# Optimization experiments

Hardware: AMD Instinct MI355X
Metric: run time of the kernel (lower is better)

Reference implementation:

```python
import jax, jax.numpy as jnp
import numpy as np

N = 100000
E = 1600000
IN_C = 128
OUT_C = 64
HID = 2 * OUT_C  # 128


def setup_inputs() -> dict:
    key = jax.random.key(0)
    k = jax.random.split(key, 6)
    x = jax.random.normal(k[0], (N, IN_C), dtype=jnp.float32)
    edge_index = jax.random.randint(k[1], (2, E), 0, N, dtype=jnp.int64)
    # GCNConv params (glorot-ish scale)
    W1 = jax.random.normal(k[2], (IN_C, HID), dtype=jnp.float32) / np.sqrt(IN_C)
    b1 = jnp.zeros((HID,), dtype=jnp.float32)
    W2 = jax.random.normal(k[3], (HID, OUT_C), dtype=jnp.float32) / np.sqrt(HID)
    b2 = jnp.zeros((OUT_C,), dtype=jnp.float32)
    return {"x": x, "edge_index": edge_index, "W1": W1, "b1": b1, "W2": W2, "b2": b2}


def _gcn_norm(edge_index, num_nodes):
    # add_self_loops=False: norm over given edges only.
    row, col = edge_index[0], edge_index[1]  # source, target
    deg = jax.ops.segment_sum(jnp.ones((edge_index.shape[1],), jnp.float32), col,
                              num_segments=num_nodes)
    dinv = jnp.where(deg > 0, 1.0 / jnp.sqrt(deg), 0.0)
    return dinv[row] * dinv[col]  # [E]


def _gcn_conv(x, edge_index, norm, W, b):
    row, col = edge_index[0], edge_index[1]
    h = x @ W                                   # [N, D_out] transform first
    msg = h[row] * norm[:, None]                # gather + scale  [E, D_out]
    agg = jax.ops.segment_sum(msg, col, num_segments=x.shape[0])  # scatter-add
    return agg + b


def reference(x, edge_index, W1, b1, W2, b2):
    # Dropout(p=0.9) is identity in eval mode (deterministic baseline).
    norm = _gcn_norm(edge_index, x.shape[0])
    h = _gcn_conv(x, edge_index, norm, W1, b1)
    h = jax.nn.relu(h)
    out = _gcn_conv(h, edge_index, norm, W2, b2)
    return out
```

## Files before the change

### kernel.cpp

```cpp
#include <hip/hip_runtime.h>

#define N_NODES 100000
#define N_EDGES 1600000
#define INC 128
#define HIDC 128
#define OUTC 64

constexpr int BSH = 9;
constexpr int BTGT = 1 << BSH;
constexpr int NBUCK = (N_NODES + BTGT - 1) / BTGT;
constexpr int BCAP = 10240;
constexpr int BIN_TILE = 2048;
constexpr int BIN_EPT = BIN_TILE / 256;
constexpr int NBINBLK = (N_EDGES + BIN_TILE - 1) / BIN_TILE;


__device__ __forceinline__ float blo(unsigned u) { return __uint_as_float(u << 16); }
__device__ __forceinline__ float bhi(unsigned u) { return __uint_as_float(u & 0xFFFF0000u); }
__device__ __forceinline__ unsigned pack_bf2(float a, float b) {
    unsigned ua = __float_as_uint(a);
    ua = (ua + 0x7FFFu + ((ua >> 16) & 1u)) >> 16;
    unsigned ub = __float_as_uint(b);
    ub = (ub + 0x7FFFu + ((ub >> 16) & 1u)) >> 16;
    return ua | (ub << 16);
}


__global__ void k_binit(int* __restrict__ bcur) {
    int b = threadIdx.x;
    if (b < NBUCK) bcur[b] = b * BCAP;
}

__global__ __launch_bounds__(256) void k_bin(const int* __restrict__ ei,
                                             int* __restrict__ bcur,
                                             unsigned* __restrict__ staging) {
    __shared__ int cnt[256];
    __shared__ int base[256];
    const int tid = threadIdx.x;
    cnt[tid] = 0;
    __syncthreads();
    const int e0 = blockIdx.x * BIN_TILE;
    unsigned pk[BIN_EPT];
    int bk[BIN_EPT];
#pragma unroll
    for (int r = 0; r < BIN_EPT; ++r) {
        int e = e0 + r * 256 + tid;
        if (e < N_EDGES) {
            int t = __builtin_nontemporal_load(ei + N_EDGES + e);
            int s = __builtin_nontemporal_load(ei + e);
            bk[r] = t >> BSH;
            pk[r] = ((unsigned)s << BSH) | (unsigned)(t & (BTGT - 1));
            atomicAdd(&cnt[bk[r]], 1);
        } else {
            bk[r] = -1;
        }
    }
    __syncthreads();
    if (tid < NBUCK) {
        int c = cnt[tid];
        base[tid] = (c > 0) ? atomicAdd(&bcur[tid], c) : 0;
    }
    __syncthreads();
#pragma unroll
    for (int r = 0; r < BIN_EPT; ++r) {
        if (bk[r] >= 0) {
            int g = atomicAdd(&base[bk[r]], 1);
            staging[g] = pk[r];
        }
    }
}

__global__ void k_bucket_scan(const int* __restrict__ bcur, int* __restrict__ bbase,
                              int* __restrict__ offs) {
    __shared__ int sdata[256];
    const int tid = threadIdx.x;
    int v = (tid < NBUCK) ? (bcur[tid] - tid * BCAP) : 0;
    sdata[tid] = v;
    __syncthreads();
    for (int off = 1; off < 256; off <<= 1) {
        int t = (tid >= off) ? sdata[tid - off] : 0;
        __syncthreads();
        sdata[tid] += t;
        __syncthreads();
    }
    if (tid < NBUCK) bbase[tid] = sdata[tid] - v;
    if (tid == 0) offs[N_NODES] = N_EDGES;
}

__global__ __launch_bounds__(256) void k_scatter2(const unsigned* __restrict__ staging,
                                                  const int* __restrict__ bcur,
                                                  const int* __restrict__ bbase,
                                                  int* __restrict__ offs,
                                                  float* __restrict__ dinv,
                                                  int* __restrict__ csr_row) {
    __shared__ int cnt[BTGT];
    __shared__ int pos[BTGT];
    __shared__ int sdata[256];
    const int b = blockIdx.x;
    const int tid = threadIdx.x;
    const int segb = b * BCAP;
    const int n = bcur[b] - segb;
    const int g0 = b << BSH;
    const int bb = bbase[b];
    cnt[tid] = 0;
    cnt[tid + 256] = 0;
    __syncthreads();
    for (int j = tid; j < n; j += 256) {
        atomicAdd(&cnt[staging[segb + j] & (BTGT - 1)], 1);
    }
    __syncthreads();
    const int c0 = cnt[2 * tid], c1 = cnt[2 * tid + 1];
    const int s = c0 + c1;
    sdata[tid] = s;
    __syncthreads();
    for (int off = 1; off < 256; off <<= 1) {
        int t = (tid >= off) ? sdata[tid - off] : 0;
        __syncthreads();
        sdata[tid] += t;
        __syncthreads();
    }
    const int texcl = sdata[tid] - s;
    const int o0 = bb + texcl;
    const int o1 = o0 + c0;
    const int gg0 = g0 + 2 * tid, gg1 = g0 + 2 * tid + 1;
    if (gg0 < N_NODES) {
        offs[gg0] = o0;
        dinv[gg0] = (c0 > 0) ? rsqrtf((float)c0) : 0.f;
    }
    if (gg1 < N_NODES) {
        offs[gg1] = o1;
        dinv[gg1] = (c1 > 0) ? rsqrtf((float)c1) : 0.f;
    }
    pos[2 * tid] = o0;
    pos[2 * tid + 1] = o1;
    __syncthreads();
    for (int j = tid; j < n; j += 256) {
        unsigned p = staging[segb + j];
        int lt = p & (BTGT - 1);
        int src = (int)(p >> BSH);
        int pp = atomicAdd(&pos[lt], 1);
        csr_row[pp] = src;
    }
}


template <int BN, int OUTTOT>
__global__ __launch_bounds__(256) void k_gemm3(const float* __restrict__ X,
                                               const float* __restrict__ W,
                                               const float* __restrict__ dinv,
                                               unsigned short* __restrict__ outb) {
    constexpr int OG = OUTTOT / 8;
    constexpr int NG = 256 / OG;
    static_assert(NG * 4 == BN, "tile mismatch");
    constexpr int KC = 32;
    constexpr int HW = OUTTOT / 2;
    constexpr int XITER = (BN * KC) / 1024;
    constexpr int WITER = (KC * OUTTOT) / 1024;

    __shared__ float xs[BN][KC + 4];
    __shared__ float wa[KC][HW];
    __shared__ float wb[KC][HW];

    const int tid = threadIdx.x;
    const int oq = tid % OG;
    const int nq = tid / OG;
    const int n0 = blockIdx.x * BN;
    float acc[4][8] = {};

    for (int kc = 0; kc < 128; kc += KC) {
#pragma unroll
        for (int m = 0; m < XITER; ++m) {
            int q = tid + 256 * m;
            int row = q / (KC / 4);
            int kq = q % (KC / 4);
            int nn = n0 + row;
            float4 v = make_float4(0.f, 0.f, 0.f, 0.f);
            if (nn < N_NODES)
                v = *reinterpret_cast<const float4*>(X + (size_t)nn * 128 + kc + kq * 4);
            *reinterpret_cast<float4*>(&xs[row][kq * 4]) = v;
        }
#pragma unroll
        for (int m = 0; m < WITER; ++m) {
            int q = tid + 256 * m;
            int row = q / (OUTTOT / 4);
            int fq = q % (OUTTOT / 4);
            float4 v = *reinterpret_cast<const float4*>(W + (size_t)(kc + row) * OUTTOT + fq * 4);
            float* dst = (fq & 1) ? &wb[row][(fq >> 1) * 4] : &wa[row][(fq >> 1) * 4];
            *reinterpret_cast<float4*>(dst) = v;
        }
        __syncthreads();
#pragma unroll 8
        for (int k = 0; k < KC; ++k) {
            const float4 w0 = *reinterpret_cast<const float4*>(&wa[k][oq * 4]);
            const float4 w1 = *reinterpret_cast<const float4*>(&wb[k][oq * 4]);
#pragma unroll
            for (int j = 0; j < 4; ++j) {
                float xv = xs[nq + NG * j][k];
                acc[j][0] += xv * w0.x;
                acc[j][1] += xv * w0.y;
                acc[j][2] += xv * w0.z;
                acc[j][3] += xv * w0.w;
                acc[j][4] += xv * w1.x;
                acc[j][5] += xv * w1.y;
                acc[j][6] += xv * w1.z;
                acc[j][7] += xv * w1.w;
            }
        }
        __syncthreads();
    }
#pragma unroll
    for (int j = 0; j < 4; ++j) {
        int nn = n0 + nq + NG * j;
        if (nn < N_NODES) {
            float s = dinv[nn];
            uint4 pkv;
            pkv.x = pack_bf2(acc[j][0] * s, acc[j][1] * s);
            pkv.y = pack_bf2(acc[j][2] * s, acc[j][3] * s);
            pkv.z = pack_bf2(acc[j][4] * s, acc[j][5] * s);
            pkv.w = pack_bf2(acc[j][6] * s, acc[j][7] * s);
            *reinterpret_cast<uint4*>(outb + (size_t)nn * OUTTOT + oq * 8) = pkv;
        }
    }
}


template <int OC, int U, bool RELU>
__global__ __launch_bounds__(256) void k_aggp(const uint4* __restrict__ hs,
                                              const int* __restrict__ csr_row,
                                              const int* __restrict__ offs,
                                              const float* __restrict__ dinv,
                                              const float* __restrict__ bias,
                                              float* __restrict__ out) {
    constexpr int LPR = (OC * 2) / 16;
    constexpr int SLOTS = 64 / LPR;
    const int lane = threadIdx.x & 63;
    const int sub = lane / LPR;
    const int q = lane % LPR;
    const int wid = (blockIdx.x * 4) + (threadIdx.x >> 6);
    const int nwaves = gridDim.x * 4;

    for (int t0 = wid * 2; t0 < N_NODES; t0 += nwaves * 2) {
        const int t1 = t0 + 1;
        const int s0 = offs[t0], e0 = offs[t0 + 1];
        const int s1 = offs[t1], e1 = offs[t1 + 1];
        float a0[8] = {}, a1[8] = {};
        int j0 = s0, j1 = s1;
        while (j0 < e0 || j1 < e1) {
            int r0[U], r1[U];
#pragma unroll
            for (int u = 0; u < U; ++u) {
                int jj = j0 + u * SLOTS + sub;
                r0[u] = (jj < e0) ? __builtin_nontemporal_load(csr_row + jj) : -1;
            }
#pragma unroll
            for (int u = 0; u < U; ++u) {
                int jj = j1 + u * SLOTS + sub;
                r1[u] = (jj < e1) ? __builtin_nontemporal_load(csr_row + jj) : -1;
            }
            uint4 v0[U], v1[U];
#pragma unroll
            for (int u = 0; u < U; ++u) {
                v0[u] = make_uint4(0u, 0u, 0u, 0u);
                if (r0[u] >= 0) v0[u] = hs[(size_t)r0[u] * LPR + q];
            }
#pragma unroll
            for (int u = 0; u < U; ++u) {
                v1[u] = make_uint4(0u, 0u, 0u, 0u);
                if (r1[u] >= 0) v1[u] = hs[(size_t)r1[u] * LPR + q];
            }
#pragma unroll
            for (int u = 0; u < U; ++u) {
                a0[0] += blo(v0[u].x); a0[1] += bhi(v0[u].x);
                a0[2] += blo(v0[u].y); a0[3] += bhi(v0[u].y);
                a0[4] += blo(v0[u].z); a0[5] += bhi(v0[u].z);
                a0[6] += blo(v0[u].w); a0[7] += bhi(v0[u].w);
                a1[0] += blo(v1[u].x); a1[1] += bhi(v1[u].x);
                a1[2] += blo(v1[u].y); a1[3] += bhi(v1[u].y);
                a1[4] += blo(v1[u].z); a1[5] += bhi(v1[u].z);
                a1[6] += blo(v1[u].w); a1[7] += bhi(v1[u].w);
            }
            j0 += U * SLOTS;
            j1 += U * SLOTS;
        }
#pragma unroll
        for (int off = 32; off >= LPR; off >>= 1) {
#pragma unroll
            for (int i = 0; i < 8; ++i) {
                a0[i] += __shfl_xor(a0[i], off);
                a1[i] += __shfl_xor(a1[i], off);
            }
        }
        if (lane < LPR) {
            const float4 b0 = *reinterpret_cast<const float4*>(bias + lane * 8);
            const float4 b1 = *reinterpret_cast<const float4*>(bias + lane * 8 + 4);
            const float d0 = dinv[t0], d1 = dinv[t1];
            float4 r0, r1, r2, r3;
            r0.x = a0[0] * d0 + b0.x; r0.y = a0[1] * d0 + b0.y;
            r0.z = a0[2] * d0 + b0.z; r0.w = a0[3] * d0 + b0.w;
            r1.x = a0[4] * d0 + b1.x; r1.y = a0[5] * d0 + b1.y;
            r1.z = a0[6] * d0 + b1.z; r1.w = a0[7] * d0 + b1.w;
            r2.x = a1[0] * d1 + b0.x; r2.y = a1[1] * d1 + b0.y;
            r2.z = a1[2] * d1 + b0.z; r2.w = a1[3] * d1 + b0.w;
            r3.x = a1[4] * d1 + b1.x; r3.y = a1[5] * d1 + b1.y;
            r3.z = a1[6] * d1 + b1.z; r3.w = a1[7] * d1 + b1.w;
            if (RELU) {
                r0.x = fmaxf(r0.x, 0.f); r0.y = fmaxf(r0.y, 0.f);
                r0.z = fmaxf(r0.z, 0.f); r0.w = fmaxf(r0.w, 0.f);
                r1.x = fmaxf(r1.x, 0.f); r1.y = fmaxf(r1.y, 0.f);
                r1.z = fmaxf(r1.z, 0.f); r1.w = fmaxf(r1.w, 0.f);
                r2.x = fmaxf(r2.x, 0.f); r2.y = fmaxf(r2.y, 0.f);
                r2.z = fmaxf(r2.z, 0.f); r2.w = fmaxf(r2.w, 0.f);
                r3.x = fmaxf(r3.x, 0.f); r3.y = fmaxf(r3.y, 0.f);
                r3.z = fmaxf(r3.z, 0.f); r3.w = fmaxf(r3.w, 0.f);
            }
            float* p0 = out + (size_t)t0 * OC + lane * 8;
            float* p1 = out + (size_t)t1 * OC + lane * 8;
            *reinterpret_cast<float4*>(p0) = r0;
            *reinterpret_cast<float4*>(p0 + 4) = r1;
            *reinterpret_cast<float4*>(p1) = r2;
            *reinterpret_cast<float4*>(p1 + 4) = r3;
        }
    }
}


extern "C" void kernel_launch(void* const* d_in, const int* in_sizes, int n_in,
                              void* d_out, int out_size, void* d_ws, size_t ws_size,
                              hipStream_t stream) {
    const float* x  = (const float*)d_in[0];
    const int*   ei = (const int*)d_in[1];
    const float* W1 = (const float*)d_in[2];
    const float* b1 = (const float*)d_in[3];
    const float* W2 = (const float*)d_in[4];
    const float* b2 = (const float*)d_in[5];
    float* out = (float*)d_out;

    char* w = (char*)d_ws;
    auto alloc = [&](size_t bytes) {
        void* p = (void*)w;
        w += (bytes + 255) & ~(size_t)255;
        return p;
    };
    float* dinv    = (float*)alloc((size_t)N_NODES * 4);
    int*   offs    = (int*)alloc((size_t)(N_NODES + 1) * 4);
    int*   bcur    = (int*)alloc((size_t)NBUCK * 4);
    int*   bbase   = (int*)alloc(256 * 4);
    unsigned* staging = (unsigned*)alloc((size_t)NBUCK * BCAP * 4);
    int*   csr_row = (int*)alloc((size_t)N_EDGES * 4);
    unsigned short* hs1 = (unsigned short*)alloc((size_t)N_NODES * HIDC * 2);
    float* h       = (float*)alloc((size_t)N_NODES * HIDC * 4);
    unsigned short* hs2 = hs1;

    k_binit<<<1, 256, 0, stream>>>(bcur);
    k_bin<<<NBINBLK, 256, 0, stream>>>(ei, bcur, staging);
    k_bucket_scan<<<1, 256, 0, stream>>>(bcur, bbase, offs);
    k_scatter2<<<NBUCK, 256, 0, stream>>>(staging, bcur, bbase, offs, dinv, csr_row);

    k_gemm3<64, HIDC><<<(N_NODES + 63) / 64, 256, 0, stream>>>(x, W1, dinv, hs1);
    k_aggp<HIDC, 4, true><<<2048, 256, 0, stream>>>((const uint4*)hs1, csr_row, offs, dinv, b1, h);

    k_gemm3<128, OUTC><<<(N_NODES + 127) / 128, 256, 0, stream>>>(h, W2, dinv, hs2);
    k_aggp<OUTC, 2, false><<<2048, 256, 0, stream>>>((const uint4*)hs2, csr_row, offs, dinv, b2, out);
}
```

Before: 335.8 us.

## Split layer-1 aggregation into feature halves and node ranges for cache locality

After: 356.0 us. 6.0% more time.

```diff
diff --git a/kernel.cpp b/kernel.cpp
--- a/kernel.cpp
+++ b/kernel.cpp
@@ -219,6 +219,124 @@
             pkv.z = pack_bf2(acc[j][4] * s, acc[j][5] * s);
             pkv.w = pack_bf2(acc[j][6] * s, acc[j][7] * s);
             *reinterpret_cast<uint4*>(outb + (size_t)nn * OUTTOT + oq * 8) = pkv;
+        }
+    }
+}
+
+
+template <bool RELU>
+__global__ __launch_bounds__(256) void k_aggs(const uint4* __restrict__ hs,
+                                              const int* __restrict__ csr_row,
+                                              const int* __restrict__ offs,
+                                              const float* __restrict__ dinv,
+                                              const float* __restrict__ bias,
+                                              float* __restrict__ out) {
+    constexpr int LPR = 8;
+    constexpr int SLOTS = 8;
+    constexpr int U = 2;
+    constexpr int NPW = 4;
+    constexpr int RQ = 16;
+    constexpr int NRANGES = 4;
+    constexpr int RLEN = N_NODES / NRANGES;
+
+    const int pass = blockIdx.x & 7;
+    const int grp = pass & 1;
+    const int rng = pass >> 1;
+    const int lo = rng * RLEN;
+    const int hi = lo + RLEN;
+    const int lane = threadIdx.x & 63;
+    const int sub = lane >> 3;
+    const int q = lane & 7;
+    const int lwid = (blockIdx.x >> 3) * 4 + (threadIdx.x >> 6);
+    const int nlw = (gridDim.x >> 3) * 4;
+
+    for (int t0 = lo + lwid * NPW; t0 < hi; t0 += nlw * NPW) {
+        int ss[NPW], ee[NPW], jj[NPW];
+#pragma unroll
+        for (int i = 0; i < NPW; ++i) {
+            ss[i] = offs[t0 + i];
+            ee[i] = offs[t0 + i + 1];
+            jj[i] = ss[i];
+        }
+        float a0[8] = {}, a1[8] = {}, a2[8] = {}, a3[8] = {};
+        bool more = true;
+        while (more) {
+            int r[NPW][U];
+#pragma unroll
+            for (int i = 0; i < NPW; ++i)
+#pragma unroll
+                for (int u = 0; u < U; ++u) {
+                    int p = jj[i] + u * SLOTS + sub;
+                    r[i][u] = (p < ee[i]) ? __builtin_nontemporal_load(csr_row + p) : -1;
+                }
+            uint4 v[NPW][U];
+#pragma unroll
+            for (int i = 0; i < NPW; ++i)
+#pragma unroll
+                for (int u = 0; u < U; ++u) {
+                    v[i][u] = make_uint4(0u, 0u, 0u, 0u);
+                    if (r[i][u] >= 0) v[i][u] = hs[(size_t)r[i][u] * RQ + grp * LPR + q];
+                }
+#pragma unroll
+            for (int u = 0; u < U; ++u) {
+                a0[0] += blo(v[0][u].x); a0[1] += bhi(v[0][u].x);
+                a0[2] += blo(v[0][u].y); a0[3] += bhi(v[0][u].y);
+                a0[4] += blo(v[0][u].z); a0[5] += bhi(v[0][u].z);
+                a0[6] += blo(v[0][u].w); a0[7] += bhi(v[0][u].w);
+                a1[0] += blo(v[1][u].x); a1[1] += bhi(v[1][u].x);
+                a1[2] += blo(v[1][u].y); a1[3] += bhi(v[1][u].y);
+                a1[4] += blo(v[1][u].z); a1[5] += bhi(v[1][u].z);
+                a1[6] += blo(v[1][u].w); a1[7] += bhi(v[1][u].w);
+                a2[0] += blo(v[2][u].x); a2[1] += bhi(v[2][u].x);
+                a2[2] += blo(v[2][u].y); a2[3] += bhi(v[2][u].y);
+                a2[4] += blo(v[2][u].z); a2[5] += bhi(v[2][u].z);
+                a2[6] += blo(v[2][u].w); a2[7] += bhi(v[2][u].w);
+                a3[0] += blo(v[3][u].x); a3[1] += bhi(v[3][u].x);
+                a3[2] += blo(v[3][u].y); a3[3] += bhi(v[3][u].y);
+                a3[4] += blo(v[3][u].z); a3[5] += bhi(v[3][u].z);
+                a3[6] += blo(v[3][u].w); a3[7] += bhi(v[3][u].w);
+            }
+            more = false;
+#pragma unroll
+            for (int i = 0; i < NPW; ++i) {
+                jj[i] += U * SLOTS;
+                more = more || (jj[i] < ee[i]);
+            }
+        }
+#pragma unroll
+        for (int off = 32; off >= LPR; off >>= 1) {
+#pragma unroll
+            for (int i = 0; i < 8; ++i) {
+                a0[i] += __shfl_xor(a0[i], off);
+                a1[i] += __shfl_xor(a1[i], off);
+                a2[i] += __shfl_xor(a2[i], off);
+                a3[i] += __shfl_xor(a3[i], off);
+            }
+        }
+        if (lane < LPR) {
+            const float* bp = bias + grp * 64 + q * 8;
+            const float4 b0 = *reinterpret_cast<const float4*>(bp);
+            const float4 b1 = *reinterpret_cast<const float4*>(bp + 4);
+            float* ap[NPW] = {a0, a1, a2, a3};
+#pragma unroll
+            for (int i = 0; i < NPW; ++i) {
+                const float dt = dinv[t0 + i];
+                float* a = ap[i];
+                float4 r0, r1;
+                r0.x = a[0] * dt + b0.x; r0.y = a[1] * dt + b0.y;
+                r0.z = a[2] * dt + b0.z; r0.w = a[3] * dt + b0.w;
+                r1.x = a[4] * dt + b1.x; r1.y = a[5] * dt + b1.y;
+                r1.z = a[6] * dt + b1.z; r1.w = a[7] * dt + b1.w;
+                if (RELU) {
+                    r0.x = fmaxf(r0.x, 0.f); r0.y = fmaxf(r0.y, 0.f);
+                    r0.z = fmaxf(r0.z, 0.f); r0.w = fmaxf(r0.w, 0.f);
+                    r1.x = fmaxf(r1.x, 0.f); r1.y = fmaxf(r1.y, 0.f);
+                    r1.z = fmaxf(r1.z, 0.f); r1.w = fmaxf(r1.w, 0.f);
+                }
+                float* po = out + (size_t)(t0 + i) * HIDC + grp * 64 + q * 8;
+                *reinterpret_cast<float4*>(po) = r0;
+                *reinterpret_cast<float4*>(po + 4) = r1;
+            }
         }
     }
 }
@@ -311,7 +429,7 @@
                 r2.x = fmaxf(r2.x, 0.f); r2.y = fmaxf(r2.y, 0.f);
                 r2.z = fmaxf(r2.z, 0.f); r2.w = fmaxf(r2.w, 0.f);
                 r3.x = fmaxf(r3.x, 0.f); r3.y = fmaxf(r3.y, 0.f);
-                r3.z = fmaxf(r3.z, 0.f); r3.w = fmaxf(r3.w, 0.f);
+                r3.w = fmaxf(r3.w, 0.f); r3.z = fmaxf(r3.z, 0.f);
             }
             float* p0 = out + (size_t)t0 * OC + lane * 8;
             float* p1 = out + (size_t)t1 * OC + lane * 8;
@@ -357,7 +475,7 @@
     k_scatter2<<<NBUCK, 256, 0, stream>>>(staging, bcur, bbase, offs, dinv, csr_row);
 
     k_gemm3<64, HIDC><<<(N_NODES + 63) / 64, 256, 0, stream>>>(x, W1, dinv, hs1);
-    k_aggp<HIDC, 4, true><<<2048, 256, 0, stream>>>((const uint4*)hs1, csr_row, offs, dinv, b1, h);
+    k_aggs<true><<<2048, 256, 0, stream>>>((const uint4*)hs1, csr_row, offs, dinv, b1, h);
 
     k_gemm3<128, OUTC><<<(N_NODES + 127) / 128, 256, 0, stream>>>(h, W2, dinv, hs2);
     k_aggp<OUTC, 2, false><<<2048, 256, 0, stream>>>((const uint4*)hs2, csr_row, offs, dinv, b2, out);
```

## Store hidden activations in bf16 and read them as bf16 in second GEMM

Applied to the files above, without the earlier changes.

After: 327.2 us. -2.5%, faster.

```diff
diff --git a/kernel.cpp b/kernel.cpp
--- a/kernel.cpp
+++ b/kernel.cpp
@@ -144,8 +144,8 @@
 }
 
 
-template <int BN, int OUTTOT>
-__global__ __launch_bounds__(256) void k_gemm3(const float* __restrict__ X,
+template <int BN, int OUTTOT, bool BF16IN>
+__global__ __launch_bounds__(256) void k_gemm4(const void* __restrict__ Xv,
                                                const float* __restrict__ W,
                                                const float* __restrict__ dinv,
                                                unsigned short* __restrict__ outb) {
@@ -154,31 +154,55 @@
     static_assert(NG * 4 == BN, "tile mismatch");
     constexpr int KC = 32;
     constexpr int HW = OUTTOT / 2;
-    constexpr int XITER = (BN * KC) / 1024;
-    constexpr int WITER = (KC * OUTTOT) / 1024;
-
-    __shared__ float xs[BN][KC + 4];
+    constexpr int PAD = KC + 1;
+
+    __shared__ float xs[BN][PAD];
     __shared__ float wa[KC][HW];
     __shared__ float wb[KC][HW];
 
     const int tid = threadIdx.x;
     const int oq = tid % OG;
     const int nq = tid / OG;
+    const int r0 = nq * 4;
     const int n0 = blockIdx.x * BN;
     float acc[4][8] = {};
 
     for (int kc = 0; kc < 128; kc += KC) {
-#pragma unroll
-        for (int m = 0; m < XITER; ++m) {
-            int q = tid + 256 * m;
-            int row = q / (KC / 4);
-            int kq = q % (KC / 4);
-            int nn = n0 + row;
-            float4 v = make_float4(0.f, 0.f, 0.f, 0.f);
-            if (nn < N_NODES)
-                v = *reinterpret_cast<const float4*>(X + (size_t)nn * 128 + kc + kq * 4);
-            *reinterpret_cast<float4*>(&xs[row][kq * 4]) = v;
-        }
+        if (BF16IN) {
+            constexpr int ITER = (BN * KC) / (256 * 8);
+            const unsigned short* X = (const unsigned short*)Xv;
+#pragma unroll
+            for (int m = 0; m < (ITER > 0 ? ITER : 1); ++m) {
+                int q = tid + 256 * m;
+                int row = q / (KC / 8);
+                int kq = q % (KC / 8);
+                int nn = n0 + row;
+                uint4 v = make_uint4(0u, 0u, 0u, 0u);
+                if (nn < N_NODES)
+                    v = *reinterpret_cast<const uint4*>(X + (size_t)nn * 128 + kc + kq * 8);
+                float* d = &xs[row][kq * 8];
+                d[0] = blo(v.x); d[1] = bhi(v.x);
+                d[2] = blo(v.y); d[3] = bhi(v.y);
+                d[4] = blo(v.z); d[5] = bhi(v.z);
+                d[6] = blo(v.w); d[7] = bhi(v.w);
+            }
+        } else {
+            constexpr int ITER = (BN * KC) / (256 * 4);
+            const float* X = (const float*)Xv;
+#pragma unroll
+            for (int m = 0; m < (ITER > 0 ? ITER : 1); ++m) {
+                int q = tid + 256 * m;
+                int row = q / (KC / 4);
+                int kq = q % (KC / 4);
+                int nn = n0 + row;
+                float4 v = make_float4(0.f, 0.f, 0.f, 0.f);
+                if (nn < N_NODES)
+                    v = *reinterpret_cast<const float4*>(X + (size_t)nn * 128 + kc + kq * 4);
+                float* d = &xs[row][kq * 4];
+                d[0] = v.x; d[1] = v.y; d[2] = v.z; d[3] = v.w;
+            }
+        }
+        constexpr int WITER = (KC * OUTTOT) / 1024;
 #pragma unroll
         for (int m = 0; m < WITER; ++m) {
             int q = tid + 256 * m;
@@ -195,7 +219,7 @@
             const float4 w1 = *reinterpret_cast<const float4*>(&wb[k][oq * 4]);
 #pragma unroll
             for (int j = 0; j < 4; ++j) {
-                float xv = xs[nq + NG * j][k];
+                float xv = xs[r0 + j][k];
                 acc[j][0] += xv * w0.x;
                 acc[j][1] += xv * w0.y;
                 acc[j][2] += xv * w0.z;
@@ -210,7 +234,7 @@
     }
 #pragma unroll
     for (int j = 0; j < 4; ++j) {
-        int nn = n0 + nq + NG * j;
+        int nn = n0 + r0 + j;
         if (nn < N_NODES) {
             float s = dinv[nn];
             uint4 pkv;
@@ -219,6 +243,91 @@
             pkv.z = pack_bf2(acc[j][4] * s, acc[j][5] * s);
             pkv.w = pack_bf2(acc[j][6] * s, acc[j][7] * s);
             *reinterpret_cast<uint4*>(outb + (size_t)nn * OUTTOT + oq * 8) = pkv;
+        }
+    }
+}
+
+
+template <int OC, int U, bool RELU, bool BF16OUT>
+__global__ __launch_bounds__(256) void k_aggv(const uint4* __restrict__ hs,
+                                              const int* __restrict__ csr_row,
+                                              const int* __restrict__ offs,
+                                              const float* __restrict__ dinv,
+                                              const float* __restrict__ bias,
+                                              void* __restrict__ outv) {
+    constexpr int LPR = (OC * 2) / 16;
+    constexpr int SLOTS = 64 / LPR;
+    const int lane = threadIdx.x & 63;
+    const int sub = lane / LPR;
+    const int q = lane % LPR;
+    const int wid = (blockIdx.x * 4) + (threadIdx.x >> 6);
+    const int nwaves = gridDim.x * 4;
+
+    for (int t = wid; t < N_NODES; t += nwaves) {
+        const int s = offs[t], e2 = offs[t + 1];
+        float acc[8] = {0.f, 0.f, 0.f, 0.f, 0.f, 0.f, 0.f, 0.f};
+        for (int j = s; j < e2; j += U * SLOTS) {
+            int rr[U];
+#pragma unroll
+            for (int u = 0; u < U; ++u) {
+                int jj = j + u * SLOTS + sub;
+                rr[u] = (jj < e2) ? __builtin_nontemporal_load(csr_row + jj) : -1;
+            }
+            uint4 vv[U];
+#pragma unroll
+            for (int u = 0; u < U; ++u) {
+                vv[u] = make_uint4(0u, 0u, 0u, 0u);
+                if (rr[u] >= 0) vv[u] = hs[(size_t)rr[u] * LPR + q];
+            }
+#pragma unroll
+            for (int u = 0; u < U; ++u) {
+                acc[0] += blo(vv[u].x);
+                acc[1] += bhi(vv[u].x);
+                acc[2] += blo(vv[u].y);
+                acc[3] += bhi(vv[u].y);
+                acc[4] += blo(vv[u].z);
+                acc[5] += bhi(vv[u].z);
+                acc[6] += blo(vv[u].w);
+                acc[7] += bhi(vv[u].w);
+            }
+        }
+#pragma unroll
+        for (int off = 32; off >= LPR; off >>= 1) {
+#pragma unroll
+            for (int i = 0; i < 8; ++i) acc[i] += __shfl_xor(acc[i], off);
+        }
+        if (lane < LPR) {
+            const float dt = dinv[t];
+            const float4 b0 = *reinterpret_cast<const float4*>(bias + lane * 8);
+            const float4 b1 = *reinterpret_cast<const float4*>(bias + lane * 8 + 4);
+            float4 r0, r1;
+            r0.x = acc[0] * dt + b0.x;
+            r0.y = acc[1] * dt + b0.y;
+            r0.z = acc[2] * dt + b0.z;
+            r0.w = acc[3] * dt + b0.w;
+            r1.x = acc[4] * dt + b1.x;
+            r1.y = acc[5] * dt + b1.y;
+            r1.z = acc[6] * dt + b1.z;
+            r1.w = acc[7] * dt + b1.w;
+            if (RELU) {
+                r0.x = fmaxf(r0.x, 0.f); r0.y = fmaxf(r0.y, 0.f);
+                r0.z = fmaxf(r0.z, 0.f); r0.w = fmaxf(r0.w, 0.f);
+                r1.x = fmaxf(r1.x, 0.f); r1.y = fmaxf(r1.y, 0.f);
+                r1.z = fmaxf(r1.z, 0.f); r1.w = fmaxf(r1.w, 0.f);
+            }
+            if (BF16OUT) {
+                unsigned short* o = (unsigned short*)outv + (size_t)t * OC + lane * 8;
+                uint4 pk;
+                pk.x = pack_bf2(r0.x, r0.y);
+                pk.y = pack_bf2(r0.z, r0.w);
+                pk.z = pack_bf2(r1.x, r1.y);
+                pk.w = pack_bf2(r1.z, r1.w);
+                *reinterpret_cast<uint4*>(o) = pk;
+            } else {
+                float* po = (float*)outv + (size_t)t * OC + lane * 8;
+                *reinterpret_cast<float4*>(po) = r0;
+                *reinterpret_cast<float4*>(po + 4) = r1;
+            }
         }
     }
 }
@@ -348,7 +457,7 @@
     unsigned* staging = (unsigned*)alloc((size_t)NBUCK * BCAP * 4);
     int*   csr_row = (int*)alloc((size_t)N_EDGES * 4);
     unsigned short* hs1 = (unsigned short*)alloc((size_t)N_NODES * HIDC * 2);
-    float* h       = (float*)alloc((size_t)N_NODES * HIDC * 4);
+    unsigned short* h   = (unsigned short*)alloc((size_t)N_NODES * HIDC * 2);
     unsigned short* hs2 = hs1;
 
     k_binit<<<1, 256, 0, stream>>>(bcur);
@@ -356,9 +465,11 @@
     k_bucket_scan<<<1, 256, 0, stream>>>(bcur, bbase, offs);
     k_scatter2<<<NBUCK, 256, 0, stream>>>(staging, bcur, bbase, offs, dinv, csr_row);
 
-    k_gemm3<64, HIDC><<<(N_NODES + 63) / 64, 256, 0, stream>>>(x, W1, dinv, hs1);
-    k_aggp<HIDC, 4, true><<<2048, 256, 0, stream>>>((const uint4*)hs1, csr_row, offs, dinv, b1, h);
-
-    k_gemm3<128, OUTC><<<(N_NODES + 127) / 128, 256, 0, stream>>>(h, W2, dinv, hs2);
-    k_aggp<OUTC, 2, false><<<2048, 256, 0, stream>>>((const uint4*)hs2, csr_row, offs, dinv, b2, out);
-}
+    k_gemm4<64, HIDC, false><<<(N_NODES + 63) / 64, 256, 0, stream>>>(x, W1, dinv, hs1);
+    k_aggv<HIDC, 4, true, true><<<2048, 256, 0, stream>>>((const uint4*)hs1, csr_row, offs,
+                                                          dinv, b1, h);
+
+    k_gemm4<128, OUTC, true><<<(N_NODES + 127) / 128, 256, 0, stream>>>(h, W2, dinv, hs2);
+    k_aggp<OUTC, 2, false><<<2048, 256, 0, stream>>>((const uint4*)hs2, csr_row, offs,
+                                                     dinv, b2, out);
+}
```
